# Optimization experiments

Measured on AMD Instinct MI355X. Metric: run time of the kernel, lower is better.

Reference implementation:

```python
import jax, jax.numpy as jnp
import numpy as np

B, S, D = 2, 2048, 1024
H, HD = 16, 64          # num_heads, head_dim (D == H*HD)
FF = 4 * D
EPS = 1e-5

def _xavier(key, shape):
    fan_out, fan_in = shape
    lim = np.sqrt(6.0 / (fan_in + fan_out))
    return jax.random.uniform(key, shape, jnp.float32, -lim, lim)

def setup_inputs() -> dict:
    key = jax.random.key(0)
    ks = jax.random.split(key, 8)
    return {
        "x": jax.random.normal(ks[0], (B, S, D), jnp.float32),
        "g1": jnp.ones((D,), jnp.float32), "b1": jnp.zeros((D,), jnp.float32),
        "Wqkv": _xavier(ks[1], (3 * D, D)), "bqkv": jnp.zeros((3 * D,), jnp.float32),
        "Wo": _xavier(ks[2], (D, D)), "bo": jnp.zeros((D,), jnp.float32),
        "g2": jnp.ones((D,), jnp.float32), "b2": jnp.zeros((D,), jnp.float32),
        "W1": _xavier(ks[3], (FF, D)), "b1m": jnp.zeros((FF,), jnp.float32),
        "W2": _xavier(ks[4], (D, FF)), "b2m": jnp.zeros((D,), jnp.float32),
    }

def _ln(x, g, b):
    m = jnp.mean(x, axis=-1, keepdims=True)
    v = jnp.var(x, axis=-1, keepdims=True)
    return (x - m) * jax.lax.rsqrt(v + EPS) * g + b

def reference(x, g1, b1, Wqkv, bqkv, Wo, bo, g2, b2, W1, b1m, W2, b2m):
    # --- pre-norm attention ---
    h = _ln(x, g1, b1)
    qkv = h @ Wqkv.T + bqkv                                  # [B,S,3D]
    qkv = qkv.reshape(B, S, H, 3 * HD).transpose(0, 2, 1, 3)  # [B,H,S,3hd]
    q, k, v = jnp.split(qkv, 3, axis=-1)                      # each [B,H,S,hd]
    scores = jnp.einsum('bhqd,bhkd->bhqk', q, k) / np.sqrt(HD).astype(np.float32)
    att = jax.nn.softmax(scores, axis=-1)                     # [B,H,S,S]
    vals = jnp.einsum('bhqk,bhkd->bhqd', att, v)
    vals = vals.transpose(0, 2, 1, 3).reshape(B, S, D)
    x = x + (vals @ Wo.T + bo)
    # --- pre-norm MLP (dropouts inactive in eval) ---
    h = _ln(x, g2, b2)
    h = jax.nn.gelu(h @ W1.T + b1m, approximate=False)
    x = x + (h @ W2.T + b2m)
    return x
```

## Files before the change

### kernel.cpp

```cpp
#include <hip/hip_runtime.h>
#include <math.h>

#define BB 2
#define SS 2048
#define DD 1024
#define HH 16
#define FFDIM 4096
#define NROWS 4096

typedef short bf16x8 __attribute__((ext_vector_type(8)));
typedef float f32x4 __attribute__((ext_vector_type(4)));

__device__ __forceinline__ unsigned short f2bf(float f) {
    unsigned u = __float_as_uint(f);
    u += 0x7fffu + ((u >> 16) & 1u);
    return (unsigned short)(u >> 16);
}

typedef __attribute__((address_space(1))) void gvoid;
typedef __attribute__((address_space(3))) void lvoid;
__device__ __forceinline__ void glds16(const void* g, void* l) {
    __builtin_amdgcn_global_load_lds((gvoid*)g, (lvoid*)l, 16, 0, 0);
}

__device__ __forceinline__ int vkey(int kloc) {
    return (kloc & ~31) + ((kloc & 12) << 1) + ((kloc & 16) >> 2);
}

__global__ __launch_bounds__(256) void ln_kernel(const float* __restrict__ x,
                                                 const float* __restrict__ g,
                                                 const float* __restrict__ b,
                                                 unsigned short* __restrict__ out) {
    int row = blockIdx.x;
    const float* xr = x + (size_t)row * DD;
    unsigned short* orow = out + (size_t)row * DD;
    int t = threadIdx.x;
    float4 v = ((const float4*)xr)[t];
    float s  = v.x + v.y + v.z + v.w;
    float s2 = v.x*v.x + v.y*v.y + v.z*v.z + v.w*v.w;
    #pragma unroll
    for (int off = 32; off > 0; off >>= 1) {
        s  += __shfl_down(s,  off);
        s2 += __shfl_down(s2, off);
    }
    __shared__ float red1[4], red2[4];
    int wid = t >> 6, lane = t & 63;
    if (lane == 0) { red1[wid] = s; red2[wid] = s2; }
    __syncthreads();
    if (t == 0) {
        float a = 0.f, a2 = 0.f;
        #pragma unroll
        for (int i = 0; i < 4; ++i) { a += red1[i]; a2 += red2[i]; }
        red1[0] = a; red2[0] = a2;
    }
    __syncthreads();
    float mean = red1[0] * (1.0f / DD);
    float var  = red2[0] * (1.0f / DD) - mean * mean;
    float rs = rsqrtf(var + 1e-5f);
    float4 gv = ((const float4*)g)[t];
    float4 bv = ((const float4*)b)[t];
    ushort4 o;
    o.x = f2bf((v.x - mean) * rs * gv.x + bv.x);
    o.y = f2bf((v.y - mean) * rs * gv.y + bv.y);
    o.z = f2bf((v.z - mean) * rs * gv.z + bv.z);
    o.w = f2bf((v.w - mean) * rs * gv.w + bv.w);
    ((ushort4*)orow)[t] = o;
}

__global__ __launch_bounds__(256) void cast4(const float* __restrict__ a, unsigned short* __restrict__ oa,
                                             const float* __restrict__ b, unsigned short* __restrict__ ob,
                                             const float* __restrict__ c, unsigned short* __restrict__ oc,
                                             const float* __restrict__ d, unsigned short* __restrict__ od) {
    int i = blockIdx.x * 256 + threadIdx.x;
    const float* src; unsigned short* dst; int off;
    if (i < 786432)       { src = a; dst = oa; off = i; }
    else if (i < 1048576) { src = b; dst = ob; off = i - 786432; }
    else if (i < 2097152) { src = c; dst = oc; off = i - 1048576; }
    else                  { src = d; dst = od; off = i - 2097152; }
    float4 v = ((const float4*)src)[off];
    ushort4 o;
    o.x = f2bf(v.x); o.y = f2bf(v.y); o.z = f2bf(v.z); o.w = f2bf(v.w);
    ((ushort4*)dst)[off] = o;
}

__global__ __launch_bounds__(256) void reduce_add(const float* __restrict__ x1,
                                                  const float* __restrict__ P0,
                                                  const float* __restrict__ P1,
                                                  const float* __restrict__ bias,
                                                  float* __restrict__ out) {
    int i = blockIdx.x * 256 + threadIdx.x;
    float4 a = ((const float4*)x1)[i];
    float4 p = ((const float4*)P0)[i];
    float4 q = ((const float4*)P1)[i];
    float4 bv = ((const float4*)bias)[i & 255];
    float4 o;
    o.x = a.x + p.x + q.x + bv.x;
    o.y = a.y + p.y + q.y + bv.y;
    o.z = a.z + p.z + q.z + bv.z;
    o.w = a.w + p.w + q.w + bv.w;
    ((float4*)out)[i] = o;
}

template<int ACT, int RES, int OUTBF, int TN, int VT, int CS, int SPLITK>
__global__ __launch_bounds__(256, 3) void gemm_nt_mfma(
    const unsigned short* __restrict__ A,
    const unsigned short* __restrict__ W,
    const float* __restrict__ bias,
    const float* __restrict__ res,
    void* __restrict__ Cout,
    void* __restrict__ Cout2,
    unsigned short* __restrict__ Vtg,
    int M, int N, int K)
{
    constexpr int MI = (TN == 128) ? 4 : 2;
    constexpr int WR = TN / 4;
    __shared__ unsigned short SMEM[128 * 64 + TN * 64];
    unsigned short* As = SMEM;
    unsigned short* Ws = SMEM + 128 * 64;
    int tid = threadIdx.x;
    int lane = tid & 63;
    int w = tid >> 6;
    int rowbase = (TN == 128) ? ((w >> 1) * 64) : (w * 32);
    int colbase = (TN == 128) ? ((w & 1) * 64) : 0;
    int bm = blockIdx.y * 128, bn = blockIdx.x * TN;
    int col16 = lane & 15, quad = lane >> 4;

    int klen = SPLITK ? (K >> 1) : K;
    int kbase = SPLITK ? ((int)blockIdx.z * klen) : 0;

    f32x4 acc[MI][4] = {};

    int lrow = lane >> 3;
    int sw = (lane & 7) ^ lrow;
    const unsigned short* Ag = A + (size_t)(bm + w * 32 + lrow) * K + sw * 8;
    const unsigned short* Wg = W + (size_t)(bn + w * WR + lrow) * K + sw * 8;

    for (int k0 = kbase; k0 < kbase + klen; k0 += 64) {
        if (k0 != kbase) __syncthreads();
        #pragma unroll
        for (int it = 0; it < 4; ++it)
            glds16(Ag + (size_t)(8 * it) * K + k0, &As[(w * 32 + 8 * it) * 64]);
        #pragma unroll
        for (int it = 0; it < WR / 8; ++it)
            glds16(Wg + (size_t)(8 * it) * K + k0, &Ws[(w * WR + 8 * it) * 64]);
        __syncthreads();
        #pragma unroll
        for (int c = 0; c < 2; ++c) {
            bf16x8 af[MI], bfr[4];
            #pragma unroll
            for (int i = 0; i < MI; ++i) {
                int m = rowbase + i * 16 + col16;
                af[i] = *(const bf16x8*)&As[m * 64 + (((c * 4 + quad) ^ (m & 7)) * 8)];
            }
            #pragma unroll
            for (int j = 0; j < 4; ++j) {
                int n = colbase + j * 16 + col16;
                bfr[j] = *(const bf16x8*)&Ws[n * 64 + (((c * 4 + quad) ^ (n & 7)) * 8)];
            }
            #pragma unroll
            for (int i = 0; i < MI; ++i)
                #pragma unroll
                for (int j = 0; j < 4; ++j)
                    acc[i][j] = __builtin_amdgcn_mfma_f32_16x16x32_bf16(af[i], bfr[j], acc[i][j], 0, 0, 0);
        }
    }

    if constexpr (SPLITK) {
        float* P = (float*)(blockIdx.z ? Cout2 : Cout);
        #pragma unroll
        for (int i = 0; i < MI; ++i) {
            #pragma unroll
            for (int j = 0; j < 4; ++j) {
                int nn = bn + colbase + j * 16 + col16;
                #pragma unroll
                for (int r = 0; r < 4; ++r) {
                    int mm = bm + rowbase + i * 16 + quad * 4 + r;
                    P[(size_t)mm * N + nn] = acc[i][j][r];
                }
            }
        }
        return;
    }

    if constexpr (CS) {
        __syncthreads();
        #pragma unroll
        for (int i = 0; i < MI; ++i) {
            #pragma unroll
            for (int j = 0; j < 4; ++j) {
                int nl = colbase + j * 16 + col16;
                float bv = bias[bn + nl];
                int c = nl >> 4;
                #pragma unroll
                for (int r = 0; r < 4; ++r) {
                    int ml = rowbase + i * 16 + quad * 4 + r;
                    float v = acc[i][j][r] + bv;
                    if (ACT) {
                        float z = v * (1.595769122f + 0.071354816f * v * v);
                        float e = __builtin_amdgcn_exp2f(-z * 1.442695041f);
                        v = v * __builtin_amdgcn_rcpf(1.0f + e);
                    }
                    SMEM[ml * 128 + ((c ^ ((ml >> 2) & 7)) << 4) + (nl & 15)] = f2bf(v);
                }
            }
        }
        __syncthreads();
        #pragma unroll
        for (int p = 0; p < 8; ++p) {
            int cid = tid + p * 256;
            int row = cid >> 4, cc = cid & 15;
            int cs2 = cc >> 1;
            bf16x8 vv = *(bf16x8*)&SMEM[row * 128 + ((cs2 ^ ((row >> 2) & 7)) << 4) + (cc & 1) * 8];
            *(bf16x8*)&((unsigned short*)Cout)[(size_t)(bm + row) * N + bn + cc * 8] = vv;
        }
        return;
    }

    bool wave_v = VT && ((((bn + colbase) >> 6) % 3) == 2);
    if constexpr (VT) __syncthreads();

    #pragma unroll
    for (int i = 0; i < MI; ++i) {
        #pragma unroll
        for (int j = 0; j < 4; ++j) {
            int nn = bn + colbase + j * 16 + col16;
            float bv = bias[nn];
            float vv[4];
            #pragma unroll
            for (int r = 0; r < 4; ++r) {
                float v = acc[i][j][r] + bv;
                if (ACT) {
                    float z = v * (1.595769122f + 0.071354816f * v * v);
                    float e = __builtin_amdgcn_exp2f(-z * 1.442695041f);
                    v = v * __builtin_amdgcn_rcpf(1.0f + e);
                }
                vv[r] = v;
            }
            int mm0 = bm + rowbase + i * 16 + quad * 4;
            if (VT && wave_v) {
                int d = j * 16 + col16;
                int kloc = rowbase + i * 16 + quad * 4;
                int vl = vkey(kloc);
                int ch = vl >> 3;
                ushort4 pk;
                pk.x = f2bf(vv[0]); pk.y = f2bf(vv[1]);
                pk.z = f2bf(vv[2]); pk.w = f2bf(vv[3]);
                *(ushort4*)&SMEM[d * 128 + ((ch ^ (d & 7)) << 3) + (vl & 7)] = pk;
            } else {
                #pragma unroll
                for (int r = 0; r < 4; ++r) {
                    int mm = mm0 + r;
                    float v = vv[r];
                    if (RES) v += res[(size_t)mm * N + nn];
                    if (OUTBF) ((unsigned short*)Cout)[(size_t)mm * N + nn] = f2bf(v);
                    else       ((float*)Cout)[(size_t)mm * N + nn] = v;
                }
            }
        }
    }

    if constexpr (VT) {
        __syncthreads();
        bool g0v = ((bn >> 6) % 3) == 2;
        bool g1v = (((bn + 64) >> 6) % 3) == 2;
        if (g0v || g1v) {
            int vcb = g0v ? 0 : 64;
            int hh = (bn + vcb) / 192;
            int bb = bm >> 11, sr = bm & 2047;
            #pragma unroll
            for (int p = 0; p < 4; ++p) {
                int cid = tid + p * 256;
                int d = cid >> 4, ch = cid & 15;
                bf16x8 vv2 = *(bf16x8*)&SMEM[d * 128 + ((ch ^ (d & 7)) << 3)];
                *(bf16x8*)&Vtg[((size_t)((bb * HH + hh) * 64 + d)) * (size_t)SS + sr + ch * 8] = vv2;
            }
        }
    }
}

__global__ __launch_bounds__(256, 2) void attn_mfma(
    const unsigned short* __restrict__ qkv,
    const unsigned short* __restrict__ Vtg,
    unsigned short* __restrict__ outb)
{
    __shared__ unsigned short Ks[128 * 64];
    __shared__ unsigned short VtL[64 * 128];
    int tid = threadIdx.x;
    int lane = tid & 63;
    int wv = tid >> 6;
    int qt = blockIdx.x, h = blockIdx.y, b = blockIdx.z;
    int col16 = lane & 15, quad = lane >> 4;

    const unsigned short* qbase = qkv + (size_t)(b * SS) * 3072;
    const unsigned short* Kg = qbase + h * 192 + 64;
    const unsigned short* Vg = Vtg + ((size_t)(b * HH + h) * 64) * (size_t)SS;

    const float C = 0.18033688011112042f;
    bf16x8 qf[2][2];
    #pragma unroll
    for (int qq = 0; qq < 2; ++qq) {
        int qrow = qt * 128 + qq * 64 + wv * 16 + col16;
        qf[qq][0] = *(const bf16x8*)&qbase[(size_t)qrow * 3072 + h * 192 + quad * 8];
        qf[qq][1] = *(const bf16x8*)&qbase[(size_t)qrow * 3072 + h * 192 + 32 + quad * 8];
        #pragma unroll
        for (int c = 0; c < 2; ++c)
            #pragma unroll
            for (int i = 0; i < 8; ++i) {
                float f = __uint_as_float(((unsigned)(unsigned short)qf[qq][c][i]) << 16) * C;
                qf[qq][c][i] = (short)f2bf(f);
            }
    }

    f32x4 o[2][4] = {};
    float lsum[2] = {0.f, 0.f};

    for (int s0 = 0; s0 < SS; s0 += 128) {
        if (s0) __syncthreads();
        #pragma unroll
        for (int p = 0; p < 4; ++p) {
            int ci = (p * 4 + wv) * 64 + lane;
            int k = ci >> 3, sk = ci & 7, qk = sk ^ (k & 7);
            glds16(Kg + (size_t)(s0 + k) * 3072 + qk * 8, &Ks[ci * 8]);
            int dv = ci >> 4, sv = ci & 15, qv = sv ^ (dv & 7);
            glds16(Vg + (size_t)dv * SS + s0 + qv * 8, &VtL[ci * 8]);
        }
        __syncthreads();

        #pragma unroll
        for (int qq = 0; qq < 2; ++qq) {
            f32x4 st[8];
            #pragma unroll
            for (int t = 0; t < 8; ++t) {
                f32x4 z = {};
                st[t] = z;
                int key = t * 16 + col16;
                #pragma unroll
                for (int c = 0; c < 2; ++c) {
                    bf16x8 kf = *(const bf16x8*)&Ks[key * 64 + (((c * 4 + quad) ^ (key & 7)) * 8)];
                    st[t] = __builtin_amdgcn_mfma_f32_16x16x32_bf16(kf, qf[qq][c], st[t], 0, 0, 0);
                }
            }

            unsigned lo[8], hi[8];
            float psum = 0.f;
            #pragma unroll
            for (int t = 0; t < 8; ++t) {
                float p0 = __builtin_amdgcn_exp2f(st[t][0]);
                float p1 = __builtin_amdgcn_exp2f(st[t][1]);
                float p2 = __builtin_amdgcn_exp2f(st[t][2]);
                float p3 = __builtin_amdgcn_exp2f(st[t][3]);
                psum += (p0 + p1) + (p2 + p3);
                lo[t] = __builtin_amdgcn_perm(__float_as_uint(p1), __float_as_uint(p0), 0x07060302u);
                hi[t] = __builtin_amdgcn_perm(__float_as_uint(p3), __float_as_uint(p2), 0x07060302u);
            }
            psum += __shfl_xor(psum, 16);
            psum += __shfl_xor(psum, 32);
            lsum[qq] += psum;

            #pragma unroll
            for (int kc = 0; kc < 4; ++kc) {
                uint4 pk;
                pk.x = lo[2 * kc]; pk.y = hi[2 * kc];
                pk.z = lo[2 * kc + 1]; pk.w = hi[2 * kc + 1];
                bf16x8 pf = *(bf16x8*)&pk;
                #pragma unroll
                for (int nt = 0; nt < 4; ++nt) {
                    int d = nt * 16 + col16;
                    bf16x8 vf = *(const bf16x8*)&VtL[d * 128 + (((kc * 4 + quad) ^ (d & 7)) * 8)];
                    o[qq][nt] = __builtin_amdgcn_mfma_f32_16x16x32_bf16(pf, vf, o[qq][nt], 0, 0, 0);
                }
            }
        }
    }

    #pragma unroll
    for (int qq = 0; qq < 2; ++qq) {
        float linv = __builtin_amdgcn_rcpf(lsum[qq]);
        float linv_r[4];
        #pragma unroll
        for (int r = 0; r < 4; ++r) linv_r[r] = __shfl(linv, quad * 4 + r);
        int orow0 = b * SS + qt * 128 + qq * 64 + wv * 16;
        #pragma unroll
        for (int r = 0; r < 4; ++r) {
            int mm = orow0 + quad * 4 + r;
            #pragma unroll
            for (int nt = 0; nt < 4; ++nt)
                outb[(size_t)mm * DD + h * 64 + nt * 16 + col16] = f2bf(o[qq][nt][r] * linv_r[r]);
        }
    }
}

extern "C" void kernel_launch(void* const* d_in, const int* in_sizes, int n_in,
                              void* d_out, int out_size, void* d_ws, size_t ws_size,
                              hipStream_t stream) {
    const float* x    = (const float*)d_in[0];
    const float* g1   = (const float*)d_in[1];
    const float* b1   = (const float*)d_in[2];
    const float* Wqkv = (const float*)d_in[3];
    const float* bqkv = (const float*)d_in[4];
    const float* Wo   = (const float*)d_in[5];
    const float* bo   = (const float*)d_in[6];
    const float* g2   = (const float*)d_in[7];
    const float* b2   = (const float*)d_in[8];
    const float* W1   = (const float*)d_in[9];
    const float* b1m  = (const float*)d_in[10];
    const float* W2   = (const float*)d_in[11];
    const float* b2m  = (const float*)d_in[12];
    float* out = (float*)d_out;

    char* wsb = (char*)d_ws;
    unsigned short* Wq_b  = (unsigned short*)(wsb);
    unsigned short* Wo_b  = (unsigned short*)(wsb + 6291456);
    unsigned short* W1_b  = (unsigned short*)(wsb + 8388608);
    unsigned short* W2_b  = (unsigned short*)(wsb + 16777216);
    unsigned short* hb    = (unsigned short*)(wsb + 25165824);
    unsigned short* qkvb  = (unsigned short*)(wsb + 33554432);
    unsigned short* attnb = (unsigned short*)(wsb + 58720256);
    float*          x1    = (float*)(wsb + 67108864);
    unsigned short* ffb   = (unsigned short*)(wsb + 83886080);
    unsigned short* Vtg   = (unsigned short*)(wsb + 83886080);
    float*          P0    = (float*)(wsb + 33554432);
    float*          P1    = (float*)(wsb + 50331648);

    cast4<<<12288, 256, 0, stream>>>(Wqkv, Wq_b, Wo, Wo_b, W1, W1_b, W2, W2_b);

    ln_kernel<<<NROWS, 256, 0, stream>>>(x, g1, b1, hb);
    gemm_nt_mfma<0,0,1,128,1,0,0><<<dim3(24, 32), 256, 0, stream>>>(hb, Wq_b, bqkv, nullptr, qkvb,
                                                                    nullptr, Vtg, NROWS, 3 * DD, DD);
    attn_mfma<<<dim3(SS / 128, HH, BB), 256, 0, stream>>>(qkvb, Vtg, attnb);
    gemm_nt_mfma<0,1,0,64,0,0,0><<<dim3(16, 32), 256, 0, stream>>>(attnb, Wo_b, bo, x, x1,
                                                                   nullptr, nullptr, NROWS, DD, DD);
    ln_kernel<<<NROWS, 256, 0, stream>>>(x1, g2, b2, hb);
    gemm_nt_mfma<1,0,1,128,0,1,0><<<dim3(32, 32), 256, 0, stream>>>(hb, W1_b, b1m, nullptr, ffb,
                                                                    nullptr, nullptr, NROWS, FFDIM, DD);
    gemm_nt_mfma<0,0,0,128,0,0,1><<<dim3(8, 32, 2), 256, 0, stream>>>(ffb, W2_b, nullptr, nullptr, P0,
                                                                      P1, nullptr, NROWS, DD, FFDIM);
    reduce_add<<<4096, 256, 0, stream>>>(x1, P0, P1, b2m, out);
}
```

Measured before the change: 327.5 us.

## Fuse LN1 with weight cast, XCD-swizzle GEMM blocks, store split-K partials in bf16

```diff
diff --git a/kernel.cpp b/kernel.cpp
--- a/kernel.cpp
+++ b/kernel.cpp
@@ -16,6 +16,9 @@
     u += 0x7fffu + ((u >> 16) & 1u);
     return (unsigned short)(u >> 16);
 }
+__device__ __forceinline__ float bf2f(unsigned short s) {
+    return __uint_as_float(((unsigned)s) << 16);
+}
 
 typedef __attribute__((address_space(1))) void gvoid;
 typedef __attribute__((address_space(3))) void lvoid;
@@ -27,11 +30,10 @@
     return (kloc & ~31) + ((kloc & 12) << 1) + ((kloc & 16) >> 2);
 }
 
-__global__ __launch_bounds__(256) void ln_kernel(const float* __restrict__ x,
-                                                 const float* __restrict__ g,
-                                                 const float* __restrict__ b,
-                                                 unsigned short* __restrict__ out) {
-    int row = blockIdx.x;
+__device__ __forceinline__ void ln_body(const float* __restrict__ x,
+                                        const float* __restrict__ g,
+                                        const float* __restrict__ b,
+                                        unsigned short* __restrict__ out, int row) {
     const float* xr = x + (size_t)row * DD;
     unsigned short* orow = out + (size_t)row * DD;
     int t = threadIdx.x;
@@ -67,11 +69,22 @@
     ((ushort4*)orow)[t] = o;
 }
 
-__global__ __launch_bounds__(256) void cast4(const float* __restrict__ a, unsigned short* __restrict__ oa,
-                                             const float* __restrict__ b, unsigned short* __restrict__ ob,
-                                             const float* __restrict__ c, unsigned short* __restrict__ oc,
-                                             const float* __restrict__ d, unsigned short* __restrict__ od) {
-    int i = blockIdx.x * 256 + threadIdx.x;
+__global__ __launch_bounds__(256) void ln_kernel(const float* __restrict__ x,
+                                                 const float* __restrict__ g,
+                                                 const float* __restrict__ b,
+                                                 unsigned short* __restrict__ out) {
+    ln_body(x, g, b, out, blockIdx.x);
+}
+
+__global__ __launch_bounds__(256) void prep_kernel(
+    const float* __restrict__ x, const float* __restrict__ g1,
+    const float* __restrict__ b1, unsigned short* __restrict__ hb,
+    const float* __restrict__ a, unsigned short* __restrict__ oa,
+    const float* __restrict__ b, unsigned short* __restrict__ ob,
+    const float* __restrict__ c, unsigned short* __restrict__ oc,
+    const float* __restrict__ d, unsigned short* __restrict__ od) {
+    if (blockIdx.x < 4096) { ln_body(x, g1, b1, hb, blockIdx.x); return; }
+    int i = (blockIdx.x - 4096) * 256 + threadIdx.x;
     const float* src; unsigned short* dst; int off;
     if (i < 786432)       { src = a; dst = oa; off = i; }
     else if (i < 1048576) { src = b; dst = ob; off = i - 786432; }
@@ -84,24 +97,24 @@
 }
 
 __global__ __launch_bounds__(256) void reduce_add(const float* __restrict__ x1,
-                                                  const float* __restrict__ P0,
-                                                  const float* __restrict__ P1,
+                                                  const unsigned short* __restrict__ P0,
+                                                  const unsigned short* __restrict__ P1,
                                                   const float* __restrict__ bias,
                                                   float* __restrict__ out) {
     int i = blockIdx.x * 256 + threadIdx.x;
     float4 a = ((const float4*)x1)[i];
-    float4 p = ((const float4*)P0)[i];
-    float4 q = ((const float4*)P1)[i];
+    ushort4 p = ((const ushort4*)P0)[i];
+    ushort4 q = ((const ushort4*)P1)[i];
     float4 bv = ((const float4*)bias)[i & 255];
     float4 o;
-    o.x = a.x + p.x + q.x + bv.x;
-    o.y = a.y + p.y + q.y + bv.y;
-    o.z = a.z + p.z + q.z + bv.z;
-    o.w = a.w + p.w + q.w + bv.w;
+    o.x = a.x + bf2f(p.x) + bf2f(q.x) + bv.x;
+    o.y = a.y + bf2f(p.y) + bf2f(q.y) + bv.y;
+    o.z = a.z + bf2f(p.z) + bf2f(q.z) + bv.z;
+    o.w = a.w + bf2f(p.w) + bf2f(q.w) + bv.w;
     ((float4*)out)[i] = o;
 }
 
-template<int ACT, int RES, int OUTBF, int TN, int VT, int CS, int SPLITK>
+template<int ACT, int RES, int OUTBF, int TN, int VT, int CS, int SPLITK, int SWZ>
 __global__ __launch_bounds__(256, 3) void gemm_nt_mfma(
     const unsigned short* __restrict__ A,
     const unsigned short* __restrict__ W,
@@ -122,11 +135,24 @@
     int w = tid >> 6;
     int rowbase = (TN == 128) ? ((w >> 1) * 64) : (w * 32);
     int colbase = (TN == 128) ? ((w & 1) * 64) : 0;
-    int bm = blockIdx.y * 128, bn = blockIdx.x * TN;
     int col16 = lane & 15, quad = lane >> 4;
 
+    int bx, by, bz;
+    if constexpr (SWZ) {
+        int nx = gridDim.x, nz = gridDim.z;
+        int bid = blockIdx.x + nx * (blockIdx.y + 32 * blockIdx.z);
+        int xcd = bid & 7;
+        int g = bid >> 3;
+        int per = nx * nz;
+        by = xcd + 8 * (g / per);
+        int r = g % per;
+        bx = r % nx;
+        bz = r / nx;
+    } else { bx = blockIdx.x; by = blockIdx.y; bz = blockIdx.z; }
+    int bm = by * 128, bn = bx * TN;
+
     int klen = SPLITK ? (K >> 1) : K;
-    int kbase = SPLITK ? ((int)blockIdx.z * klen) : 0;
+    int kbase = SPLITK ? (bz * klen) : 0;
 
     f32x4 acc[MI][4] = {};
 
@@ -166,7 +192,7 @@
     }
 
     if constexpr (SPLITK) {
-        float* P = (float*)(blockIdx.z ? Cout2 : Cout);
+        unsigned short* P = (unsigned short*)(bz ? Cout2 : Cout);
         #pragma unroll
         for (int i = 0; i < MI; ++i) {
             #pragma unroll
@@ -175,7 +201,7 @@
                 #pragma unroll
                 for (int r = 0; r < 4; ++r) {
                     int mm = bm + rowbase + i * 16 + quad * 4 + r;
-                    P[(size_t)mm * N + nn] = acc[i][j][r];
+                    P[(size_t)mm * N + nn] = f2bf(acc[i][j][r]);
                 }
             }
         }
@@ -278,7 +304,7 @@
     }
 }
 
-__global__ __launch_bounds__(256, 2) void attn_mfma(
+__global__ __launch_bounds__(256, 3) void attn_mfma(
     const unsigned short* __restrict__ qkv,
     const unsigned short* __restrict__ Vtg,
     unsigned short* __restrict__ outb)
@@ -419,21 +445,20 @@
     float*          x1    = (float*)(wsb + 67108864);
     unsigned short* ffb   = (unsigned short*)(wsb + 83886080);
     unsigned short* Vtg   = (unsigned short*)(wsb + 83886080);
-    float*          P0    = (float*)(wsb + 33554432);
-    float*          P1    = (float*)(wsb + 50331648);
-
-    cast4<<<12288, 256, 0, stream>>>(Wqkv, Wq_b, Wo, Wo_b, W1, W1_b, W2, W2_b);
-
-    ln_kernel<<<NROWS, 256, 0, stream>>>(x, g1, b1, hb);
-    gemm_nt_mfma<0,0,1,128,1,0,0><<<dim3(24, 32), 256, 0, stream>>>(hb, Wq_b, bqkv, nullptr, qkvb,
-                                                                    nullptr, Vtg, NROWS, 3 * DD, DD);
+    unsigned short* P0    = (unsigned short*)(wsb + 33554432);
+    unsigned short* P1    = (unsigned short*)(wsb + 41943040);
+
+    prep_kernel<<<16384, 256, 0, stream>>>(x, g1, b1, hb,
+                                           Wqkv, Wq_b, Wo, Wo_b, W1, W1_b, W2, W2_b);
+    gemm_nt_mfma<0,0,1,128,1,0,0,1><<<dim3(24, 32), 256, 0, stream>>>(hb, Wq_b, bqkv, nullptr, qkvb,
+                                                                      nullptr, Vtg, NROWS, 3 * DD, DD);
     attn_mfma<<<dim3(SS / 128, HH, BB), 256, 0, stream>>>(qkvb, Vtg, attnb);
-    gemm_nt_mfma<0,1,0,64,0,0,0><<<dim3(16, 32), 256, 0, stream>>>(attnb, Wo_b, bo, x, x1,
-                                                                   nullptr, nullptr, NROWS, DD, DD);
+    gemm_nt_mfma<0,1,0,64,0,0,0,1><<<dim3(16, 32), 256, 0, stream>>>(attnb, Wo_b, bo, x, x1,
+                                                                     nullptr, nullptr, NROWS, DD, DD);
     ln_kernel<<<NROWS, 256, 0, stream>>>(x1, g2, b2, hb);
-    gemm_nt_mfma<1,0,1,128,0,1,0><<<dim3(32, 32), 256, 0, stream>>>(hb, W1_b, b1m, nullptr, ffb,
-                                                                    nullptr, nullptr, NROWS, FFDIM, DD);
-    gemm_nt_mfma<0,0,0,128,0,0,1><<<dim3(8, 32, 2), 256, 0, stream>>>(ffb, W2_b, nullptr, nullptr, P0,
-                                                                      P1, nullptr, NROWS, DD, FFDIM);
+    gemm_nt_mfma<1,0,1,128,0,1,0,1><<<dim3(32, 32), 256, 0, stream>>>(hb, W1_b, b1m, nullptr, ffb,
+                                                                      nullptr, nullptr, NROWS, FFDIM, DD);
+    gemm_nt_mfma<0,0,0,128,0,0,1,1><<<dim3(8, 32, 2), 256, 0, stream>>>(ffb, W2_b, nullptr, nullptr, P0,
+                                                                        P1, nullptr, NROWS, DD, FFDIM);
     reduce_add<<<4096, 256, 0, stream>>>(x1, P0, P1, b2m, out);
 }
```

Result: faster. 313.8 us (-4.2%).
